# Kernel optimization log

Hardware: AMD Instinct MI355X
Metric: run time of the kernel (lower is better)

The kernel has to match this reference:

```python
import jax, jax.numpy as jnp
import numpy as np

B, S, D, H, WIDTH = 4, 1024, 1024, 16, 32
DEPTH = D // H


def _build_graph(size, width, seed=0):
    # Faithful vectorized port of sparse_attention_graph
    rng = np.random.default_rng(seed)
    normal_pulls = rng.normal(0.0, 1.0 / size, (size, width // 2)) * (size * 1.3)
    nums = normal_pulls.astype(np.int32)
    positions = nums % size
    rows = np.repeat(np.arange(size), width // 2)
    cols = (positions.reshape(-1) + rows) % size
    adjm = np.zeros((size, size), dtype=np.float32)
    adjm[rows, cols] = 1.0
    adjm = np.clip(adjm + adjm.T, a_min=None, a_max=1.0)
    return jnp.asarray(adjm)


def setup_inputs() -> dict:
    key = jax.random.key(0)
    ks = jax.random.split(key, 10)
    inp = {
        'v': jax.random.normal(ks[0], (B, S, D), jnp.float32),
        'q': jax.random.normal(ks[1], (B, S, D), jnp.float32),
        'k': jax.random.normal(ks[2], (B, S, D), jnp.float32),
        'mask': jax.random.randint(ks[3], (B, 1, S, S), 0, 2, jnp.int32),
        'G': _build_graph(D, WIDTH),
        'wq': jax.random.normal(ks[4], (D, D), jnp.float32) * 0.02,
        'bq': jnp.zeros((D,), jnp.float32),
        'wk': jax.random.normal(ks[5], (D, D), jnp.float32) * 0.02,
        'bk': jnp.zeros((D,), jnp.float32),
        'wv': jax.random.normal(ks[6], (D, D), jnp.float32) * 0.02,
        'bv': jnp.zeros((D,), jnp.float32),
        'wo': jax.random.normal(ks[7], (D, D), jnp.float32) * 0.02,
        'bo': jnp.zeros((D,), jnp.float32),
    }
    return inp


def _split_heads(x):
    # [B,S,D] -> [B,H,S,depth]
    b = x.shape[0]
    return x.reshape(b, -1, H, DEPTH).transpose(0, 2, 1, 3)


def reference(v, q, k, mask, G, wq, bq, wk, bk, wv, bv, wo, bo):
    qh = _split_heads(q @ wq + bq)   # [B,H,S,dp]
    kh = _split_heads(k @ wk + bk)
    vh = _split_heads(v @ wv + bv)
    # kg = K^T @ G : [B,H,dp,S]
    kg = jnp.einsum('bhsd,st->bhdt', kh, G)
    # qkg = Q @ kg : [B,H,S,S]
    s = jnp.einsum('bhsd,bhdt->bhst', qh, kg) / jnp.sqrt(jnp.float32(DEPTH))
    s = s - 100000.0 * mask.astype(s.dtype)
    attn_weights = jax.nn.softmax(s, axis=-1)
    attn = jnp.einsum('bhst,bhtd->bhsd', attn_weights, vh)
    attn = attn.transpose(0, 2, 1, 3).reshape(q.shape[0], -1, D)
    output = attn @ wo + bo
    return (output, attn_weights)
```

## Files before the change

kernel.cpp:

```cpp
#include <hip/hip_runtime.h>
#include <cstdint>
#include <cstddef>

#define AS1 __attribute__((address_space(1)))
#define AS3 __attribute__((address_space(3)))

typedef __bf16 bf16x8 __attribute__((ext_vector_type(8)));
typedef __bf16 bf16x4 __attribute__((ext_vector_type(4)));
typedef float  f32x4  __attribute__((ext_vector_type(4)));

namespace {

constexpr int NB = 4;
constexpr int S  = 1024;
constexpr int D  = 1024;
constexpr int NH = 16;
constexpr int DP = 64;

__global__ void __launch_bounds__(256) split_k(const float* __restrict__ src,
                                               __bf16* __restrict__ hi,
                                               __bf16* __restrict__ lo,
                                               size_t n4) {
  size_t i = (size_t)blockIdx.x * blockDim.x + threadIdx.x;
  const size_t stride = (size_t)gridDim.x * blockDim.x;
  for (; i < n4; i += stride) {
    const float4 v = ((const float4*)src)[i];
    bf16x4 h;
    h[0] = (__bf16)v.x; h[1] = (__bf16)v.y; h[2] = (__bf16)v.z; h[3] = (__bf16)v.w;
    ((bf16x4*)hi)[i] = h;
    if (lo != nullptr) {
      bf16x4 l;
      l[0] = (__bf16)(v.x - (float)h[0]);
      l[1] = (__bf16)(v.y - (float)h[1]);
      l[2] = (__bf16)(v.z - (float)h[2]);
      l[3] = (__bf16)(v.w - (float)h[3]);
      ((bf16x4*)lo)[i] = l;
    }
  }
}

__global__ void __launch_bounds__(256) tsplit_k(const float* __restrict__ src,
                                                __bf16* __restrict__ hi,
                                                __bf16* __restrict__ lo,
                                                int R, int C) {
  __shared__ float tile[32][33];
  const int z = blockIdx.z;
  const float* sp = src + (size_t)z * R * C;
  __bf16* hp = hi + (size_t)z * R * C;
  __bf16* lp = lo + (size_t)z * R * C;
  const int r0 = blockIdx.y * 32, c0 = blockIdx.x * 32;
  const int tx = threadIdx.x, ty = threadIdx.y;
  #pragma unroll
  for (int rr = ty; rr < 32; rr += 8)
    tile[rr][tx] = sp[(size_t)(r0 + rr) * C + c0 + tx];
  __syncthreads();
  #pragma unroll
  for (int cc = ty; cc < 32; cc += 8) {
    const float v = tile[tx][cc];
    const __bf16 h = (__bf16)v;
    const size_t o = (size_t)(c0 + cc) * R + r0 + tx;
    hp[o] = h;
    lp[o] = (__bf16)(v - (float)h);
  }
}

__global__ void __launch_bounds__(256) softmax_k(float* __restrict__ aw) {
  const size_t row = blockIdx.x;
  float* p = aw + row * 1024;
  const int tid = threadIdx.x;
  float4 v = ((const float4*)p)[tid];
  float m = fmaxf(fmaxf(v.x, v.y), fmaxf(v.z, v.w));
  #pragma unroll
  for (int off = 32; off > 0; off >>= 1) m = fmaxf(m, __shfl_xor(m, off));
  __shared__ float red[8];
  const int wv = tid >> 6, ln = tid & 63;
  if (ln == 0) red[wv] = m;
  __syncthreads();
  m = fmaxf(fmaxf(red[0], red[1]), fmaxf(red[2], red[3]));
  const float e0 = __expf(v.x - m), e1 = __expf(v.y - m);
  const float e2 = __expf(v.z - m), e3 = __expf(v.w - m);
  float s = (e0 + e1) + (e2 + e3);
  #pragma unroll
  for (int off = 32; off > 0; off >>= 1) s += __shfl_xor(s, off);
  if (ln == 0) red[4 + wv] = s;
  __syncthreads();
  s = (red[4] + red[5]) + (red[6] + red[7]);
  const float inv = 1.0f / s;
  float4 o; o.x = e0 * inv; o.y = e1 * inv; o.z = e2 * inv; o.w = e3 * inv;
  ((float4*)p)[tid] = o;
}

struct GemmArgs {
  const void*   Ah; const void* Al;
  const __bf16* Bh; const __bf16* Bl;
  float* C; const float* bias; const int* mask;
  int M, N, K, ZH;
  long long lda, ldb, ldc;
  long long sAb, sAh, sBb, sBh, sCb, sCh, sMb;
};

template<int BM, int BN, int WM, int WN, bool A_LO, bool B_LO, bool A_F32, int EPI>
__global__ void __launch_bounds__(WM * WN * 64) gemm_k(GemmArgs g) {
  constexpr int NW = WM * WN, NT = NW * 64, BK = 32;
  constexpr int WMsz = BM / WM, WNsz = BN / WN;
  constexpr int FM = WMsz / 16, FN = WNsz / 16;
  static_assert((BM * BK / 8) % NT == 0 && (BN * BK / 8) % NT == 0, "stage divisibility");

  __shared__ __attribute__((aligned(16))) __bf16 Ash[BM * BK];
  __shared__ __attribute__((aligned(16))) __bf16 Asl[A_LO ? BM * BK : 8];
  __shared__ __attribute__((aligned(16))) __bf16 Bsh[BN * BK];
  __shared__ __attribute__((aligned(16))) __bf16 Bsl[B_LO ? BN * BK : 8];

  const int tid = threadIdx.x, wave = tid >> 6, lane = tid & 63;
  const int z = blockIdx.z;
  const int zb = z / g.ZH, zh = z - zb * g.ZH;

  const float*  Af = A_F32 ? (const float*)g.Ah + (size_t)zb * g.sAb + (size_t)zh * g.sAh : nullptr;
  const __bf16* Ah = !A_F32 ? (const __bf16*)g.Ah + (size_t)zb * g.sAb + (size_t)zh * g.sAh : nullptr;
  const __bf16* Al = A_LO  ? (const __bf16*)g.Al + (size_t)zb * g.sAb + (size_t)zh * g.sAh : nullptr;
  const __bf16* Bh = g.Bh + (size_t)zb * g.sBb + (size_t)zh * g.sBh;
  const __bf16* Bl = B_LO ? g.Bl + (size_t)zb * g.sBb + (size_t)zh * g.sBh : nullptr;
  float* C = g.C + (size_t)zb * g.sCb + (size_t)zh * g.sCh;
  const int* mk = (EPI == 2) ? g.mask + (size_t)zb * g.sMb : nullptr;

  const int m0 = blockIdx.y * BM, n0 = blockIdx.x * BN;
  const int wm = wave / WN, wn = wave % WN;
  const int lc = lane & 15;
  const int lkb = (lane >> 4) * 8;
  const int lr4 = (lane >> 4) * 4;

  f32x4 acc[FM][FN] = {};

  for (int k0 = 0; k0 < g.K; k0 += BK) {
    if constexpr (A_F32) {
      constexpr int ITF = (BM * BK / 4) / NT;
      #pragma unroll
      for (int i = 0; i < ITF; ++i) {
        const int f = i * NT + tid;
        const int row = f >> 3, c4 = f & 7;
        const float4 v = *(const float4*)(Af + (size_t)(m0 + row) * g.lda + k0 + c4 * 4);
        bf16x4 h;
        h[0] = (__bf16)v.x; h[1] = (__bf16)v.y; h[2] = (__bf16)v.z; h[3] = (__bf16)v.w;
        *(bf16x4*)&Ash[row * BK + c4 * 4] = h;
      }
    } else {
      constexpr int ITA = (BM * BK / 8) / NT;
      #pragma unroll
      for (int i = 0; i < ITA; ++i) {
        const int cb = (i * NW + wave) * 64;
        const int ch = cb + lane;
        const int row = ch >> 2, c8 = ch & 3;
        const size_t go = (size_t)(m0 + row) * g.lda + k0 + c8 * 8;
        __builtin_amdgcn_global_load_lds((AS1 void*)(Ah + go),
                                         (AS3 void*)(&Ash[cb * 8]), 16, 0, 0);
        if constexpr (A_LO)
          __builtin_amdgcn_global_load_lds((AS1 void*)(Al + go),
                                           (AS3 void*)(&Asl[cb * 8]), 16, 0, 0);
      }
    }
    {
      constexpr int ITB = (BN * BK / 8) / NT;
      #pragma unroll
      for (int i = 0; i < ITB; ++i) {
        const int cb = (i * NW + wave) * 64;
        const int ch = cb + lane;
        const int row = ch >> 2, c8 = ch & 3;
        const size_t go = (size_t)(n0 + row) * g.ldb + k0 + c8 * 8;
        __builtin_amdgcn_global_load_lds((AS1 void*)(Bh + go),
                                         (AS3 void*)(&Bsh[cb * 8]), 16, 0, 0);
        if constexpr (B_LO)
          __builtin_amdgcn_global_load_lds((AS1 void*)(Bl + go),
                                           (AS3 void*)(&Bsl[cb * 8]), 16, 0, 0);
      }
    }
    __syncthreads();

    bf16x8 ah[FM], al[FM], bh[FN], bl[FN];
    #pragma unroll
    for (int i = 0; i < FM; ++i) {
      const int r = wm * WMsz + i * 16 + lc;
      ah[i] = *(const bf16x8*)&Ash[r * BK + lkb];
      if constexpr (A_LO) al[i] = *(const bf16x8*)&Asl[r * BK + lkb];
    }
    #pragma unroll
    for (int j = 0; j < FN; ++j) {
      const int r = wn * WNsz + j * 16 + lc;
      bh[j] = *(const bf16x8*)&Bsh[r * BK + lkb];
      if constexpr (B_LO) bl[j] = *(const bf16x8*)&Bsl[r * BK + lkb];
    }
    #pragma unroll
    for (int i = 0; i < FM; ++i)
      #pragma unroll
      for (int j = 0; j < FN; ++j) {
        acc[i][j] = __builtin_amdgcn_mfma_f32_16x16x32_bf16(ah[i], bh[j], acc[i][j], 0, 0, 0);
        if constexpr (B_LO)
          acc[i][j] = __builtin_amdgcn_mfma_f32_16x16x32_bf16(ah[i], bl[j], acc[i][j], 0, 0, 0);
        if constexpr (A_LO)
          acc[i][j] = __builtin_amdgcn_mfma_f32_16x16x32_bf16(al[i], bh[j], acc[i][j], 0, 0, 0);
      }
    __syncthreads();
  }

  #pragma unroll
  for (int i = 0; i < FM; ++i)
    #pragma unroll
    for (int j = 0; j < FN; ++j)
      #pragma unroll
      for (int r = 0; r < 4; ++r) {
        const int row = m0 + wm * WMsz + i * 16 + lr4 + r;
        const int col = n0 + wn * WNsz + j * 16 + lc;
        float val = acc[i][j][r];
        if constexpr (EPI == 1) val += g.bias[col];
        if constexpr (EPI == 2) val = val * 0.125f - 100000.0f * (float)mk[(size_t)row * g.N + col];
        C[(size_t)row * g.ldc + col] = val;
      }
}

}

extern "C" void kernel_launch(void* const* d_in, const int* in_sizes, int n_in,
                              void* d_out, int out_size, void* d_ws, size_t ws_size,
                              hipStream_t stream) {
  (void)in_sizes; (void)n_in; (void)out_size; (void)ws_size;

  const float* v_in = (const float*)d_in[0];
  const float* q_in = (const float*)d_in[1];
  const float* k_in = (const float*)d_in[2];
  const int*   mask = (const int*)d_in[3];
  const float* Gm   = (const float*)d_in[4];
  const float* wq = (const float*)d_in[5];  const float* bq = (const float*)d_in[6];
  const float* wk = (const float*)d_in[7];  const float* bk = (const float*)d_in[8];
  const float* wv = (const float*)d_in[9];  const float* bv = (const float*)d_in[10];
  const float* wo = (const float*)d_in[11]; const float* bo = (const float*)d_in[12];

  float* out = (float*)d_out;
  float* aw  = out + (size_t)NB * S * D;

  char* ws = (char*)d_ws;
  auto BF = [&](size_t mb) { return (__bf16*)(ws + (mb << 20)); };
  auto FP = [&](size_t mb) { return (float*)(ws + (mb << 20)); };

  const size_t BSD = (size_t)NB * S * D;
  const dim3 tb(32, 8);

  split_k<<<2048, 256, 0, stream>>>(q_in, BF(0),  BF(8),  BSD / 4);
  split_k<<<2048, 256, 0, stream>>>(k_in, BF(16), BF(24), BSD / 4);
  split_k<<<2048, 256, 0, stream>>>(v_in, BF(32), BF(40), BSD / 4);
  split_k<<<1024, 256, 0, stream>>>(Gm, BF(112), nullptr, (size_t)S * S / 4);
  tsplit_k<<<dim3(32, 32, 1), tb, 0, stream>>>(wq, BF(48), BF(50), D, D);
  tsplit_k<<<dim3(32, 32, 1), tb, 0, stream>>>(wk, BF(52), BF(54), D, D);
  tsplit_k<<<dim3(32, 32, 1), tb, 0, stream>>>(wv, BF(56), BF(58), D, D);
  tsplit_k<<<dim3(32, 32, 1), tb, 0, stream>>>(wo, BF(60), BF(62), D, D);

  GemmArgs pa{};
  pa.M = NB * S; pa.N = D; pa.K = D; pa.ZH = 1;
  pa.lda = D; pa.ldb = D; pa.ldc = D;
  pa.Ah = BF(0);  pa.Al = BF(8);  pa.Bh = BF(48); pa.Bl = BF(50); pa.C = FP(64); pa.bias = bq;
  gemm_k<128, 128, 2, 2, true, true, false, 1><<<dim3(8, 32, 1), 256, 0, stream>>>(pa);
  pa.Ah = BF(16); pa.Al = BF(24); pa.Bh = BF(52); pa.Bl = BF(54); pa.C = FP(80); pa.bias = bk;
  gemm_k<128, 128, 2, 2, true, true, false, 1><<<dim3(8, 32, 1), 256, 0, stream>>>(pa);
  pa.Ah = BF(32); pa.Al = BF(40); pa.Bh = BF(56); pa.Bl = BF(58); pa.C = FP(96); pa.bias = bv;
  gemm_k<128, 128, 2, 2, true, true, false, 1><<<dim3(8, 32, 1), 256, 0, stream>>>(pa);

  split_k<<<2048, 256, 0, stream>>>(FP(64), BF(0), BF(8), BSD / 4);
  tsplit_k<<<dim3(32, 32, NB), tb, 0, stream>>>(FP(80), BF(16), BF(24), S, D);
  tsplit_k<<<dim3(32, 32, NB), tb, 0, stream>>>(FP(96), BF(32), BF(40), S, D);

  GemmArgs ka{};
  ka.M = S; ka.N = D; ka.K = S; ka.ZH = 1;
  ka.lda = S; ka.ldb = S; ka.ldc = D;
  ka.sBb = (long long)D * S; ka.sCb = (long long)S * D;
  ka.Ah = BF(112); ka.Bh = BF(16); ka.Bl = BF(24); ka.C = FP(80);
  gemm_k<128, 128, 2, 2, false, true, false, 0><<<dim3(8, 8, NB), 256, 0, stream>>>(ka);
  split_k<<<2048, 256, 0, stream>>>(FP(80), BF(64), BF(72), BSD / 4);

  GemmArgs sa{};
  sa.M = S; sa.N = S; sa.K = DP; sa.ZH = NH;
  sa.lda = D; sa.ldb = D; sa.ldc = S;
  sa.sAb = (long long)S * D; sa.sAh = DP;
  sa.sBb = (long long)S * D; sa.sBh = DP;
  sa.sCb = (long long)NH * S * S; sa.sCh = (long long)S * S;
  sa.sMb = (long long)S * S;
  sa.Ah = BF(0); sa.Al = BF(8); sa.Bh = BF(64); sa.Bl = BF(72); sa.C = aw; sa.mask = mask;
  gemm_k<128, 128, 2, 2, true, true, false, 2><<<dim3(8, 8, NB * NH), 256, 0, stream>>>(sa);

  softmax_k<<<NB * NH * S, 256, 0, stream>>>(aw);

  GemmArgs va{};
  va.M = S; va.N = DP; va.K = S; va.ZH = NH;
  va.lda = S; va.ldb = S; va.ldc = D;
  va.sAb = (long long)NH * S * S; va.sAh = (long long)S * S;
  va.sBb = (long long)D * S;      va.sBh = (long long)DP * S;
  va.sCb = (long long)S * D;      va.sCh = DP;
  va.Ah = aw; va.Bh = BF(32); va.Bl = BF(40); va.C = FP(96);
  gemm_k<128, 64, 2, 2, false, true, true, 0><<<dim3(1, 8, NB * NH), 256, 0, stream>>>(va);

  split_k<<<2048, 256, 0, stream>>>(FP(96), BF(114), BF(122), BSD / 4);
  GemmArgs fa{};
  fa.M = NB * S; fa.N = D; fa.K = D; fa.ZH = 1;
  fa.lda = D; fa.ldb = D; fa.ldc = D;
  fa.Ah = BF(114); fa.Al = BF(122); fa.Bh = BF(60); fa.Bl = BF(62); fa.C = out; fa.bias = bo;
  gemm_k<128, 128, 2, 2, true, true, false, 1><<<dim3(8, 32, 1), 256, 0, stream>>>(fa);
}
```

Baseline: 907.5 us.

## Fuse bf16 hi/lo splitting into GEMM epilogues and batch input conversions

GEMM epilogues now write bf16 hi/lo pairs directly, including a transposed layout for K and V. This removes the separate split and transpose passes over fp32 intermediates. The softmax also emits a bf16 copy of the attention weights, so the PV GEMM loads bf16 through the async LDS path instead of converting fp32 inline. The input and weight conversions are merged into single launches. The cost is scattered bf16 stores in the epilogues and an extra 128MB bf16 write in softmax.

New measurement: 865.7 us. 4.6% less time.

```diff
diff --git a/kernel.cpp b/kernel.cpp
--- a/kernel.cpp
+++ b/kernel.cpp
@@ -39,32 +39,57 @@
   }
 }
 
-__global__ void __launch_bounds__(256) tsplit_k(const float* __restrict__ src,
-                                                __bf16* __restrict__ hi,
-                                                __bf16* __restrict__ lo,
-                                                int R, int C) {
+__global__ void __launch_bounds__(256) split3_k(const float* __restrict__ s0,
+                                                const float* __restrict__ s1,
+                                                const float* __restrict__ s2,
+                                                __bf16* __restrict__ hi0, size_t n4) {
+  const float* srcs[3] = {s0, s1, s2};
+  const float* src = srcs[blockIdx.z];
+  __bf16* hi = hi0 + (size_t)blockIdx.z * 8388608;
+  __bf16* lo = hi + 4194304;
+  size_t i = (size_t)blockIdx.x * blockDim.x + threadIdx.x;
+  const size_t stride = (size_t)gridDim.x * blockDim.x;
+  for (; i < n4; i += stride) {
+    const float4 v = ((const float4*)src)[i];
+    bf16x4 h, l;
+    h[0] = (__bf16)v.x; h[1] = (__bf16)v.y; h[2] = (__bf16)v.z; h[3] = (__bf16)v.w;
+    l[0] = (__bf16)(v.x - (float)h[0]);
+    l[1] = (__bf16)(v.y - (float)h[1]);
+    l[2] = (__bf16)(v.z - (float)h[2]);
+    l[3] = (__bf16)(v.w - (float)h[3]);
+    ((bf16x4*)hi)[i] = h;
+    ((bf16x4*)lo)[i] = l;
+  }
+}
+
+__global__ void __launch_bounds__(256) tsplit4_k(const float* __restrict__ s0,
+                                                 const float* __restrict__ s1,
+                                                 const float* __restrict__ s2,
+                                                 const float* __restrict__ s3,
+                                                 __bf16* __restrict__ hi0) {
   __shared__ float tile[32][33];
-  const int z = blockIdx.z;
-  const float* sp = src + (size_t)z * R * C;
-  __bf16* hp = hi + (size_t)z * R * C;
-  __bf16* lp = lo + (size_t)z * R * C;
+  const float* srcs[4] = {s0, s1, s2, s3};
+  const float* sp = srcs[blockIdx.z];
+  __bf16* hp = hi0 + (size_t)blockIdx.z * 2097152;
+  __bf16* lp = hp + 1048576;
   const int r0 = blockIdx.y * 32, c0 = blockIdx.x * 32;
   const int tx = threadIdx.x, ty = threadIdx.y;
   #pragma unroll
   for (int rr = ty; rr < 32; rr += 8)
-    tile[rr][tx] = sp[(size_t)(r0 + rr) * C + c0 + tx];
+    tile[rr][tx] = sp[(size_t)(r0 + rr) * D + c0 + tx];
   __syncthreads();
   #pragma unroll
   for (int cc = ty; cc < 32; cc += 8) {
     const float v = tile[tx][cc];
     const __bf16 h = (__bf16)v;
-    const size_t o = (size_t)(c0 + cc) * R + r0 + tx;
+    const size_t o = (size_t)(c0 + cc) * D + r0 + tx;
     hp[o] = h;
     lp[o] = (__bf16)(v - (float)h);
   }
 }
 
-__global__ void __launch_bounds__(256) softmax_k(float* __restrict__ aw) {
+__global__ void __launch_bounds__(256) softmax_k(float* __restrict__ aw,
+                                                 __bf16* __restrict__ awh) {
   const size_t row = blockIdx.x;
   float* p = aw + row * 1024;
   const int tid = threadIdx.x;
@@ -88,18 +113,21 @@
   const float inv = 1.0f / s;
   float4 o; o.x = e0 * inv; o.y = e1 * inv; o.z = e2 * inv; o.w = e3 * inv;
   ((float4*)p)[tid] = o;
+  bf16x4 hb;
+  hb[0] = (__bf16)o.x; hb[1] = (__bf16)o.y; hb[2] = (__bf16)o.z; hb[3] = (__bf16)o.w;
+  ((bf16x4*)(awh + row * 1024))[tid] = hb;
 }
 
 struct GemmArgs {
-  const void*   Ah; const void* Al;
-  const __bf16* Bh; const __bf16* Bl;
-  float* C; const float* bias; const int* mask;
-  int M, N, K, ZH;
+  const __bf16 *Ah, *Al, *Bh, *Bl;
+  float* C; __bf16* Chi; __bf16* Clo;
+  const float* bias; const int* mask;
+  int N, K, ZH;
   long long lda, ldb, ldc;
   long long sAb, sAh, sBb, sBh, sCb, sCh, sMb;
 };
 
-template<int BM, int BN, int WM, int WN, bool A_LO, bool B_LO, bool A_F32, int EPI>
+template<int BM, int BN, int WM, int WN, bool A_LO, bool B_LO, int EPI>
 __global__ void __launch_bounds__(WM * WN * 64) gemm_k(GemmArgs g) {
   constexpr int NW = WM * WN, NT = NW * 64, BK = 32;
   constexpr int WMsz = BM / WM, WNsz = BN / WN;
@@ -115,12 +143,15 @@
   const int z = blockIdx.z;
   const int zb = z / g.ZH, zh = z - zb * g.ZH;
 
-  const float*  Af = A_F32 ? (const float*)g.Ah + (size_t)zb * g.sAb + (size_t)zh * g.sAh : nullptr;
-  const __bf16* Ah = !A_F32 ? (const __bf16*)g.Ah + (size_t)zb * g.sAb + (size_t)zh * g.sAh : nullptr;
-  const __bf16* Al = A_LO  ? (const __bf16*)g.Al + (size_t)zb * g.sAb + (size_t)zh * g.sAh : nullptr;
+  const __bf16* Ah = g.Ah + (size_t)zb * g.sAb + (size_t)zh * g.sAh;
+  const __bf16* Al = A_LO ? g.Al + (size_t)zb * g.sAb + (size_t)zh * g.sAh : nullptr;
   const __bf16* Bh = g.Bh + (size_t)zb * g.sBb + (size_t)zh * g.sBh;
   const __bf16* Bl = B_LO ? g.Bl + (size_t)zb * g.sBb + (size_t)zh * g.sBh : nullptr;
-  float* C = g.C + (size_t)zb * g.sCb + (size_t)zh * g.sCh;
+  float* C = (EPI == 0 || EPI == 2) ? g.C + (size_t)zb * g.sCb + (size_t)zh * g.sCh : nullptr;
+  __bf16* Chi = (EPI == 3) ? g.Chi + (size_t)zb * g.sCb + (size_t)zh * g.sCh
+                           : g.Chi;
+  __bf16* Clo = (EPI == 3) ? g.Clo + (size_t)zb * g.sCb + (size_t)zh * g.sCh
+                           : g.Clo;
   const int* mk = (EPI == 2) ? g.mask + (size_t)zb * g.sMb : nullptr;
 
   const int m0 = blockIdx.y * BM, n0 = blockIdx.x * BN;
@@ -132,18 +163,7 @@
   f32x4 acc[FM][FN] = {};
 
   for (int k0 = 0; k0 < g.K; k0 += BK) {
-    if constexpr (A_F32) {
-      constexpr int ITF = (BM * BK / 4) / NT;
-      #pragma unroll
-      for (int i = 0; i < ITF; ++i) {
-        const int f = i * NT + tid;
-        const int row = f >> 3, c4 = f & 7;
-        const float4 v = *(const float4*)(Af + (size_t)(m0 + row) * g.lda + k0 + c4 * 4);
-        bf16x4 h;
-        h[0] = (__bf16)v.x; h[1] = (__bf16)v.y; h[2] = (__bf16)v.z; h[3] = (__bf16)v.w;
-        *(bf16x4*)&Ash[row * BK + c4 * 4] = h;
-      }
-    } else {
+    {
       constexpr int ITA = (BM * BK / 8) / NT;
       #pragma unroll
       for (int i = 0; i < ITA; ++i) {
@@ -204,16 +224,52 @@
   #pragma unroll
   for (int i = 0; i < FM; ++i)
     #pragma unroll
-    for (int j = 0; j < FN; ++j)
+    for (int j = 0; j < FN; ++j) {
+      const int row = m0 + wm * WMsz + i * 16 + lr4;
+      const int col = n0 + wn * WNsz + j * 16 + lc;
+      float v[4];
       #pragma unroll
-      for (int r = 0; r < 4; ++r) {
-        const int row = m0 + wm * WMsz + i * 16 + lr4 + r;
-        const int col = n0 + wn * WNsz + j * 16 + lc;
-        float val = acc[i][j][r];
-        if constexpr (EPI == 1) val += g.bias[col];
-        if constexpr (EPI == 2) val = val * 0.125f - 100000.0f * (float)mk[(size_t)row * g.N + col];
-        C[(size_t)row * g.ldc + col] = val;
-      }
+      for (int r = 0; r < 4; ++r) v[r] = acc[i][j][r];
+      if constexpr (EPI != 2) {
+        if (g.bias != nullptr) {
+          const float b = g.bias[col];
+          #pragma unroll
+          for (int r = 0; r < 4; ++r) v[r] += b;
+        }
+      }
+      if constexpr (EPI == 0) {
+        #pragma unroll
+        for (int r = 0; r < 4; ++r)
+          C[(size_t)(row + r) * g.ldc + col] = v[r];
+      }
+      if constexpr (EPI == 2) {
+        #pragma unroll
+        for (int r = 0; r < 4; ++r)
+          C[(size_t)(row + r) * g.ldc + col] =
+              v[r] * 0.125f - 100000.0f * (float)mk[(size_t)(row + r) * g.N + col];
+      }
+      if constexpr (EPI == 3) {
+        #pragma unroll
+        for (int r = 0; r < 4; ++r) {
+          const __bf16 h = (__bf16)v[r];
+          const size_t o = (size_t)(row + r) * g.ldc + col;
+          Chi[o] = h;
+          Clo[o] = (__bf16)(v[r] - (float)h);
+        }
+      }
+      if constexpr (EPI == 4) {
+        bf16x4 h4, l4;
+        #pragma unroll
+        for (int r = 0; r < 4; ++r) {
+          h4[r] = (__bf16)v[r];
+          l4[r] = (__bf16)(v[r] - (float)h4[r]);
+        }
+        const size_t b = (size_t)(row >> 10), rr = row & 1023;
+        const size_t o = b * g.sCb + (size_t)col * g.ldc + rr;
+        *(bf16x4*)&Chi[o] = h4;
+        *(bf16x4*)&Clo[o] = l4;
+      }
+    }
 }
 
 }
@@ -238,67 +294,62 @@
 
   char* ws = (char*)d_ws;
   auto BF = [&](size_t mb) { return (__bf16*)(ws + (mb << 20)); };
-  auto FP = [&](size_t mb) { return (float*)(ws + (mb << 20)); };
 
   const size_t BSD = (size_t)NB * S * D;
-  const dim3 tb(32, 8);
-
-  split_k<<<2048, 256, 0, stream>>>(q_in, BF(0),  BF(8),  BSD / 4);
-  split_k<<<2048, 256, 0, stream>>>(k_in, BF(16), BF(24), BSD / 4);
-  split_k<<<2048, 256, 0, stream>>>(v_in, BF(32), BF(40), BSD / 4);
+
+  split3_k<<<dim3(1024, 1, 3), 256, 0, stream>>>(q_in, k_in, v_in, BF(0), BSD / 4);
   split_k<<<1024, 256, 0, stream>>>(Gm, BF(112), nullptr, (size_t)S * S / 4);
-  tsplit_k<<<dim3(32, 32, 1), tb, 0, stream>>>(wq, BF(48), BF(50), D, D);
-  tsplit_k<<<dim3(32, 32, 1), tb, 0, stream>>>(wk, BF(52), BF(54), D, D);
-  tsplit_k<<<dim3(32, 32, 1), tb, 0, stream>>>(wv, BF(56), BF(58), D, D);
-  tsplit_k<<<dim3(32, 32, 1), tb, 0, stream>>>(wo, BF(60), BF(62), D, D);
+  tsplit4_k<<<dim3(32, 32, 4), dim3(32, 8), 0, stream>>>(wq, wk, wv, wo, BF(48));
 
   GemmArgs pa{};
-  pa.M = NB * S; pa.N = D; pa.K = D; pa.ZH = 1;
+  pa.N = D; pa.K = D; pa.ZH = 1;
   pa.lda = D; pa.ldb = D; pa.ldc = D;
-  pa.Ah = BF(0);  pa.Al = BF(8);  pa.Bh = BF(48); pa.Bl = BF(50); pa.C = FP(64); pa.bias = bq;
-  gemm_k<128, 128, 2, 2, true, true, false, 1><<<dim3(8, 32, 1), 256, 0, stream>>>(pa);
-  pa.Ah = BF(16); pa.Al = BF(24); pa.Bh = BF(52); pa.Bl = BF(54); pa.C = FP(80); pa.bias = bk;
-  gemm_k<128, 128, 2, 2, true, true, false, 1><<<dim3(8, 32, 1), 256, 0, stream>>>(pa);
-  pa.Ah = BF(32); pa.Al = BF(40); pa.Bh = BF(56); pa.Bl = BF(58); pa.C = FP(96); pa.bias = bv;
-  gemm_k<128, 128, 2, 2, true, true, false, 1><<<dim3(8, 32, 1), 256, 0, stream>>>(pa);
-
-  split_k<<<2048, 256, 0, stream>>>(FP(64), BF(0), BF(8), BSD / 4);
-  tsplit_k<<<dim3(32, 32, NB), tb, 0, stream>>>(FP(80), BF(16), BF(24), S, D);
-  tsplit_k<<<dim3(32, 32, NB), tb, 0, stream>>>(FP(96), BF(32), BF(40), S, D);
+  pa.Ah = BF(0);  pa.Al = BF(8);  pa.Bh = BF(48); pa.Bl = BF(50);
+  pa.Chi = BF(64); pa.Clo = BF(72); pa.bias = bq;
+  gemm_k<128, 128, 2, 2, true, true, 3><<<dim3(8, 32, 1), 256, 0, stream>>>(pa);
+  pa.Ah = BF(16); pa.Al = BF(24); pa.Bh = BF(52); pa.Bl = BF(54);
+  pa.Chi = BF(80); pa.Clo = BF(88); pa.bias = bk;
+  pa.ldc = S; pa.sCb = (long long)D * S;
+  gemm_k<128, 128, 2, 2, true, true, 4><<<dim3(8, 32, 1), 256, 0, stream>>>(pa);
+  pa.Ah = BF(32); pa.Al = BF(40); pa.Bh = BF(56); pa.Bl = BF(58);
+  pa.Chi = BF(96); pa.Clo = BF(104); pa.bias = bv;
+  gemm_k<128, 128, 2, 2, true, true, 4><<<dim3(8, 32, 1), 256, 0, stream>>>(pa);
 
   GemmArgs ka{};
-  ka.M = S; ka.N = D; ka.K = S; ka.ZH = 1;
+  ka.N = D; ka.K = S; ka.ZH = 1;
   ka.lda = S; ka.ldb = S; ka.ldc = D;
   ka.sBb = (long long)D * S; ka.sCb = (long long)S * D;
-  ka.Ah = BF(112); ka.Bh = BF(16); ka.Bl = BF(24); ka.C = FP(80);
-  gemm_k<128, 128, 2, 2, false, true, false, 0><<<dim3(8, 8, NB), 256, 0, stream>>>(ka);
-  split_k<<<2048, 256, 0, stream>>>(FP(80), BF(64), BF(72), BSD / 4);
+  ka.Ah = BF(112); ka.Bh = BF(80); ka.Bl = BF(88);
+  ka.Chi = BF(114); ka.Clo = BF(122); ka.bias = nullptr;
+  gemm_k<128, 128, 2, 2, false, true, 3><<<dim3(8, 8, NB), 256, 0, stream>>>(ka);
 
   GemmArgs sa{};
-  sa.M = S; sa.N = S; sa.K = DP; sa.ZH = NH;
+  sa.N = S; sa.K = DP; sa.ZH = NH;
   sa.lda = D; sa.ldb = D; sa.ldc = S;
   sa.sAb = (long long)S * D; sa.sAh = DP;
   sa.sBb = (long long)S * D; sa.sBh = DP;
   sa.sCb = (long long)NH * S * S; sa.sCh = (long long)S * S;
   sa.sMb = (long long)S * S;
-  sa.Ah = BF(0); sa.Al = BF(8); sa.Bh = BF(64); sa.Bl = BF(72); sa.C = aw; sa.mask = mask;
-  gemm_k<128, 128, 2, 2, true, true, false, 2><<<dim3(8, 8, NB * NH), 256, 0, stream>>>(sa);
-
-  softmax_k<<<NB * NH * S, 256, 0, stream>>>(aw);
+  sa.Ah = BF(64); sa.Al = BF(72); sa.Bh = BF(114); sa.Bl = BF(122);
+  sa.C = aw; sa.mask = mask;
+  gemm_k<128, 128, 2, 2, true, true, 2><<<dim3(8, 8, NB * NH), 256, 0, stream>>>(sa);
+
+  softmax_k<<<NB * NH * S, 256, 0, stream>>>(aw, BF(146));
 
   GemmArgs va{};
-  va.M = S; va.N = DP; va.K = S; va.ZH = NH;
+  va.N = DP; va.K = S; va.ZH = NH;
   va.lda = S; va.ldb = S; va.ldc = D;
   va.sAb = (long long)NH * S * S; va.sAh = (long long)S * S;
   va.sBb = (long long)D * S;      va.sBh = (long long)DP * S;
   va.sCb = (long long)S * D;      va.sCh = DP;
-  va.Ah = aw; va.Bh = BF(32); va.Bl = BF(40); va.C = FP(96);
-  gemm_k<128, 64, 2, 2, false, true, true, 0><<<dim3(1, 8, NB * NH), 256, 0, stream>>>(va);
-
-  split_k<<<2048, 256, 0, stream>>>(FP(96), BF(114), BF(122), BSD / 4);
+  va.Ah = BF(146); va.Bh = BF(96); va.Bl = BF(104);
+  va.Chi = BF(130); va.Clo = BF(138); va.bias = nullptr;
+  gemm_k<128, 64, 2, 2, false, true, 3><<<dim3(1, 8, NB * NH), 256, 0, stream>>>(va);
+
   GemmArgs fa{};
-  fa.M = NB * S; fa.N = D; fa.K = D; fa.ZH = 1;
+  fa.N = D; fa.K = D; fa.ZH = 1;
   fa.lda = D; fa.ldb = D; fa.ldc = D;
-  fa.Ah = BF(114); fa.Al = BF(122); fa.Bh = BF(60); fa.Bl = BF(62); fa.C = out; fa.bias = bo;
-  gemm_k<128, 128, 2, 2, true, true, false, 1><<<dim3(8, 32, 1), 256, 0, stream>>>(fa);
-}
+  fa.Ah = BF(130); fa.Al = BF(138); fa.Bh = BF(60); fa.Bl = BF(62);
+  fa.C = out; fa.bias = bo;
+  gemm_k<128, 128, 2, 2, true, true, 0><<<dim3(8, 32, 1), 256, 0, stream>>>(fa);
+}
```
